# Kernel optimization log

Measured on AMD Instinct MI355X. Metric: run time of the kernel, lower is better.

Reference implementation:

```python
import jax, jax.numpy as jnp
import numpy as np

# CPC 'same'-mode InfoNCE loss. encoded_x/context: [S, B, L] (steps, batch, latent).
# predictor(context, k) is modeled as a per-k linear map with weight Wk[k] of shape [L, L]
# (y = x @ Wk[k].T), the standard CPC prediction head.

def setup_inputs() -> dict:
    key = jax.random.key(0)
    k1, k2, k3 = jax.random.split(key, 3)
    S, B, L, K = 128, 256, 512, 8
    encoded_x = jax.random.normal(k1, (S, B, L), dtype=jnp.float32)
    context = jax.random.normal(k2, (S, B, L), dtype=jnp.float32)
    Wk = jax.random.normal(k3, (K, L, L), dtype=jnp.float32) * (1.0 / np.sqrt(L))
    return {
        "encoded_x": encoded_x,
        "context": context,
        "Wk": Wk,
        "timesteps_in": 16,
        "timesteps_out": 8,
        "timesteps_ignore": 0,
    }


def reference(encoded_x, context, Wk, timesteps_in, timesteps_out, timesteps_ignore):
    S, B, L = encoded_x.shape
    K = timesteps_out
    # number of inner 'step' iterations: context[T_in : -(K + ignore + 1)]
    steps = S - timesteps_in - (K + timesteps_ignore + 1)
    ctx = context[timesteps_in:timesteps_in + steps]            # [steps, B, L]
    # predictor for all k at once: pred[k, s, b, :] = ctx[s, b] @ Wk[k].T
    pred = jnp.einsum('sbl,kml->ksbm', ctx, Wk)                 # [K, steps, B, L]
    # encoded_latent for each k: encoded_x[T_in + k + 1 : T_in + k + 1 + steps]
    idx = timesteps_in + 1 + jnp.arange(K)[:, None] + jnp.arange(steps)[None, :]
    enc = encoded_x[idx]                                        # [K, steps, B, L]
    # sim[k, s, b, c] = <enc[k,s,b], pred[k,s,c]>  (== mm(enc, pred.T) per (k, step))
    sim = jnp.einsum('ksbl,kscl->ksbc', enc, pred)              # [K, steps, B, B]
    logp = jax.nn.log_softmax(sim, axis=-1)                     # LogSoftmax(dim=-1)
    # loss: sum of diagonals, normalized by -(B * K * steps)
    diag_sum = jnp.einsum('ksbb->', logp)
    denom = B * K * steps
    loss = diag_sum / (-1.0 * denom)
    # correct: argmax over dim 0 (rows, enc axis) per column == arange(B)
    pred_cls = jnp.argmax(logp, axis=2)                         # [K, steps, B]
    correct = jnp.sum(pred_cls == jnp.arange(B)[None, None, :])
    accuracy = correct.astype(jnp.float32) / denom
    return (accuracy, loss)
```

## Files before the change

### kernel.cpp

```cpp
#include <hip/hip_runtime.h>
#include <math.h>
#include <stdint.h>

#define S_DIM 128
#define B_DIM 256
#define L_DIM 512
#define K_DIM 8
#define T_IN  16
#define STEPS 103
#define DENOM (K_DIM * STEPS * B_DIM)
#define PRED_K ((size_t)STEPS * B_DIM * L_DIM)

typedef __attribute__((ext_vector_type(8))) short short8;
typedef __attribute__((ext_vector_type(4))) float f32x4;

__device__ __forceinline__ short f2bf(float f) {
    unsigned u = __float_as_uint(f);
    u += 0x7FFFu + ((u >> 16) & 1u);
    return (short)(u >> 16);
}

__device__ __forceinline__ void load_lds16(const void* g, void* l) {
    __builtin_amdgcn_global_load_lds(
        (const __attribute__((address_space(1))) unsigned*)g,
        (__attribute__((address_space(3))) unsigned*)l, 16, 0, 0);
}

#define ENC4 ((S_DIM * B_DIM * L_DIM) / 4)
#define CTX4 ((STEPS * B_DIM * L_DIM) / 4)
#define WK4  ((K_DIM * L_DIM * L_DIM) / 4)
#define CV_N (ENC4 + CTX4 + WK4)
#define Z_N  (DENOM + 2)
__global__ void convert_all(const float* __restrict__ enc_in, const float* __restrict__ ctx_in,
                            const float* __restrict__ wk_in, short* __restrict__ enc_out,
                            short* __restrict__ ctx_out, short* __restrict__ wk_out,
                            unsigned long long* __restrict__ zbuf) {
    for (int i = blockIdx.x * blockDim.x + threadIdx.x; i < CV_N + Z_N;
         i += gridDim.x * blockDim.x) {
        if (i >= CV_N) { zbuf[i - CV_N] = 0ull; continue; }
        const float4* src; short4* dst; int j;
        if (i < ENC4)             { src = (const float4*)enc_in; dst = (short4*)enc_out; j = i; }
        else if (i < ENC4 + CTX4) { src = (const float4*)ctx_in; dst = (short4*)ctx_out; j = i - ENC4; }
        else                      { src = (const float4*)wk_in;  dst = (short4*)wk_out;  j = i - ENC4 - CTX4; }
        const float4 v = src[j];
        short4 o;
        o.x = f2bf(v.x); o.y = f2bf(v.y); o.z = f2bf(v.z); o.w = f2bf(v.w);
        dst[j] = o;
    }
}

__global__ __launch_bounds__(256)
void gemm_bf16(const short* __restrict__ A, const short* __restrict__ W,
               short* __restrict__ C) {
    __shared__ short As[128 * 64];
    __shared__ short Bs[128 * 64];
    const int gx  = gridDim.x;
    const int nwg = gx * gridDim.y;
    const int id  = blockIdx.y * gx + blockIdx.x;
    const int q8 = nwg >> 3, r8 = nwg & 7;
    const int xcd = id & 7;
    const int lin = (xcd < r8 ? xcd * (q8 + 1) : r8 * (q8 + 1) + (xcd - r8) * q8)
                  + (id >> 3);
    const int lgx = 31 - __clz(gx);
    const int bm = lin >> lgx;
    const int xc = lin & (gx - 1);
    const int kin = xc >> 2, cn = xc & 3;

    const int t = threadIdx.x;
    const int w = t >> 6, lane = t & 63, quad = lane >> 4, l15 = lane & 15;
    const int wm = w & 1, wn = w >> 1;
    const int rl8 = lane >> 3, ch8 = lane & 7;

    const short* Ab = A + (size_t)bm * 128 * L_DIM;
    const short* Wb = W + ((size_t)kin * L_DIM + cn * 128) * L_DIM;
    short* Ck = C + kin * PRED_K;

    f32x4 acc[4][4] = {};

    for (int kt = 0; kt < L_DIM; kt += 64) {
        #pragma unroll
        for (int q = 0; q < 4; q++) {
            const int rb = w * 32 + q * 8;
            const int row = rb + rl8;
            const int ch = ch8 ^ (row & 7);
            load_lds16(Ab + (size_t)row * L_DIM + kt + ch * 8, &As[rb * 64]);
            load_lds16(Wb + (size_t)row * L_DIM + kt + ch * 8, &Bs[rb * 64]);
        }
        __syncthreads();
        #pragma unroll
        for (int k2 = 0; k2 < 2; k2++) {
            short8 a[4], b[4];
            #pragma unroll
            for (int i = 0; i < 4; i++) {
                const int m = wm * 64 + i * 16 + l15;
                a[i] = *(const short8*)&As[m * 64 + ((k2 * 4 + quad) ^ (m & 7)) * 8];
                const int n = wn * 64 + i * 16 + l15;
                b[i] = *(const short8*)&Bs[n * 64 + ((k2 * 4 + quad) ^ (n & 7)) * 8];
            }
            #pragma unroll
            for (int i = 0; i < 4; i++)
                #pragma unroll
                for (int j = 0; j < 4; j++)
                    acc[i][j] = __builtin_amdgcn_mfma_f32_16x16x32_bf16(a[i], b[j], acc[i][j], 0, 0, 0);
        }
        __syncthreads();
    }
    #pragma unroll
    for (int i = 0; i < 4; i++)
        #pragma unroll
        for (int r = 0; r < 4; r++) {
            const int row = bm * 128 + wm * 64 + i * 16 + quad * 4 + r;
            short* Cr = Ck + (size_t)row * L_DIM + cn * 128 + wn * 64 + l15;
            #pragma unroll
            for (int j = 0; j < 4; j++)
                Cr[j * 16] = f2bf(acc[i][j][r]);
        }
}

__global__ __launch_bounds__(512, 2)
void sim_phase(const short* __restrict__ encbf, const short* __restrict__ pred,
               const int k0, unsigned long long* __restrict__ col_best,
               float* __restrict__ diag_accum) {
    __shared__ short Es[2][256 * 64];
    __shared__ short Ps[2][256 * 64];
    __shared__ float rmx[256][2];
    __shared__ float rsx[256][2];
    __shared__ float dred[8];
    const int s = blockIdx.x, kin = blockIdx.y;
    const int k = k0 + kin;
    const int t = threadIdx.x, w = t >> 6, lane = t & 63;
    const int quad = lane >> 4, l15 = lane & 15;
    const int wm = w & 3, wn = w >> 2;
    const int rl8 = lane >> 3, ch8 = lane & 7;

    const short* Eb = encbf + ((size_t)(T_IN + 1 + k + s) * B_DIM) * L_DIM;
    const short* Pb = pred + kin * PRED_K + (size_t)s * B_DIM * L_DIM;

    const short* esrc[4]; const short* psrc[4]; int rdst[4];
    #pragma unroll
    for (int q = 0; q < 4; q++) {
        const int rb = w * 32 + q * 8, row = rb + rl8;
        const int co = (ch8 ^ (row & 7)) * 8;
        esrc[q] = Eb + (size_t)row * L_DIM + co;
        psrc[q] = Pb + (size_t)row * L_DIM + co;
        rdst[q] = rb * 64;
    }

    #pragma unroll
    for (int q = 0; q < 4; q++) load_lds16(esrc[q], &Es[0][rdst[q]]);
    #pragma unroll
    for (int q = 0; q < 4; q++) load_lds16(psrc[q], &Ps[0][rdst[q]]);
    __syncthreads();

    f32x4 acc[4][8] = {};
    int cur = 0;
    #pragma unroll
    for (int kt = 0; kt < L_DIM; kt += 64) {
        if (kt + 64 < L_DIM) {
            #pragma unroll
            for (int q = 0; q < 4; q++)
                load_lds16(esrc[q] + kt + 64, &Es[cur ^ 1][rdst[q]]);
            #pragma unroll
            for (int q = 0; q < 4; q++)
                load_lds16(psrc[q] + kt + 64, &Ps[cur ^ 1][rdst[q]]);
        }
        #pragma unroll
        for (int k2 = 0; k2 < 2; k2++) {
            short8 a[4], b[8];
            #pragma unroll
            for (int i = 0; i < 4; i++) {
                const int m = wm * 64 + i * 16 + l15;
                a[i] = *(const short8*)&Es[cur][m * 64 + ((k2 * 4 + quad) ^ (m & 7)) * 8];
            }
            #pragma unroll
            for (int j = 0; j < 8; j++) {
                const int n = wn * 128 + j * 16 + l15;
                b[j] = *(const short8*)&Ps[cur][n * 64 + ((k2 * 4 + quad) ^ (n & 7)) * 8];
            }
            #pragma unroll
            for (int i = 0; i < 4; i++)
                #pragma unroll
                for (int j = 0; j < 8; j++)
                    acc[i][j] = __builtin_amdgcn_mfma_f32_16x16x32_bf16(a[i], b[j], acc[i][j], 0, 0, 0);
        }
        __syncthreads();
        cur ^= 1;
    }

    float rm[4][4];
    #pragma unroll
    for (int i = 0; i < 4; i++)
        #pragma unroll
        for (int r = 0; r < 4; r++) {
            float m = acc[i][0][r];
            #pragma unroll
            for (int j = 1; j < 8; j++) m = fmaxf(m, acc[i][j][r]);
            rm[i][r] = m;
        }
    #pragma unroll
    for (int off = 1; off < 16; off <<= 1)
        #pragma unroll
        for (int i = 0; i < 4; i++)
            #pragma unroll
            for (int r = 0; r < 4; r++)
                rm[i][r] = fmaxf(rm[i][r], __shfl_xor(rm[i][r], off, 64));
    if (l15 == 0)
        #pragma unroll
        for (int i = 0; i < 4; i++)
            #pragma unroll
            for (int r = 0; r < 4; r++)
                rmx[wm * 64 + i * 16 + quad * 4 + r][wn] = rm[i][r];
    __syncthreads();

    float mrow[4][4];
    #pragma unroll
    for (int i = 0; i < 4; i++)
        #pragma unroll
        for (int r = 0; r < 4; r++) {
            const float2 v = *(const float2*)rmx[wm * 64 + i * 16 + quad * 4 + r];
            mrow[i][r] = fmaxf(v.x, v.y);
        }

    float rs[4][4];
    #pragma unroll
    for (int i = 0; i < 4; i++)
        #pragma unroll
        for (int r = 0; r < 4; r++) {
            float sum = 0.f;
            #pragma unroll
            for (int j = 0; j < 8; j++) sum += __expf(acc[i][j][r] - mrow[i][r]);
            rs[i][r] = sum;
        }
    #pragma unroll
    for (int off = 1; off < 16; off <<= 1)
        #pragma unroll
        for (int i = 0; i < 4; i++)
            #pragma unroll
            for (int r = 0; r < 4; r++)
                rs[i][r] += __shfl_xor(rs[i][r], off, 64);
    if (l15 == 0)
        #pragma unroll
        for (int i = 0; i < 4; i++)
            #pragma unroll
            for (int r = 0; r < 4; r++)
                rsx[wm * 64 + i * 16 + quad * 4 + r][wn] = rs[i][r];
    __syncthreads();

    float lse[4][4];
    #pragma unroll
    for (int i = 0; i < 4; i++)
        #pragma unroll
        for (int r = 0; r < 4; r++) {
            const float2 v = *(const float2*)rsx[wm * 64 + i * 16 + quad * 4 + r];
            lse[i][r] = mrow[i][r] + __logf(v.x + v.y);
        }

    #pragma unroll
    for (int j = 0; j < 8; j++) {
        unsigned long long best = 0;
        #pragma unroll
        for (int i = 0; i < 4; i++)
            #pragma unroll
            for (int r = 0; r < 4; r++) {
                const int grow = wm * 64 + i * 16 + quad * 4 + r;
                const float v = acc[i][j][r] - lse[i][r];
                unsigned int fb = __float_as_uint(v);
                fb = (fb & 0x80000000u) ? ~fb : (fb | 0x80000000u);
                const unsigned long long p =
                    ((unsigned long long)fb << 32) | (unsigned long long)(255 - grow);
                if (p > best) best = p;
            }
        unsigned long long o;
        o = __shfl_xor(best, 16, 64); if (o > best) best = o;
        o = __shfl_xor(best, 32, 64); if (o > best) best = o;
        if (quad == 0)
            atomicMax(&col_best[((size_t)k * STEPS + s) * B_DIM + wn * 128 + j * 16 + l15], best);
    }

    {
        float dv = 0.f;
        #pragma unroll
        for (int i = 0; i < 4; i++)
            #pragma unroll
            for (int j = 0; j < 8; j++)
                #pragma unroll
                for (int r = 0; r < 4; r++) {
                    const int grow = wm * 64 + i * 16 + quad * 4 + r;
                    const int c = wn * 128 + j * 16 + l15;
                    if (grow == c) dv += acc[i][j][r] - lse[i][r];
                }
        #pragma unroll
        for (int off = 1; off < 64; off <<= 1) dv += __shfl_xor(dv, off, 64);
        if (lane == 0) dred[w] = dv;
    }
    __syncthreads();
    if (t == 0) {
        float dv = 0.f;
        #pragma unroll
        for (int i = 0; i < 8; i++) dv += dred[i];
        atomicAdd(diag_accum, dv);
    }
}

__global__ void count_finalize(const unsigned long long* __restrict__ col_best,
                               int* __restrict__ correct_accum,
                               float* __restrict__ diag_accum,
                               unsigned int* __restrict__ done,
                               float* __restrict__ out) {
    __shared__ int red[256];
    const int t = threadIdx.x;
    int cnt = 0;
    for (int i = blockIdx.x * 256 + t; i < DENOM; i += gridDim.x * 256) {
        const int c = i & (B_DIM - 1);
        const int b = 255 - (int)(col_best[i] & 0xFFFFFFFFull);
        cnt += (b == c) ? 1 : 0;
    }
    red[t] = cnt;
    __syncthreads();
    for (int off = 128; off > 0; off >>= 1) {
        if (t < off) red[t] += red[t + off];
        __syncthreads();
    }
    if (t == 0) {
        atomicAdd(correct_accum, red[0]);
        __threadfence();
        if (atomicAdd(done, 1u) == gridDim.x - 1) {
            const int   c = atomicAdd(correct_accum, 0);
            const float d = atomicAdd(diag_accum, 0.0f);
            const float denom = (float)DENOM;
            out[0] = (float)c / denom;
            out[1] = -d / denom;
        }
    }
}

extern "C" void kernel_launch(void* const* d_in, const int* in_sizes, int n_in,
                              void* d_out, int out_size, void* d_ws, size_t ws_size,
                              hipStream_t stream) {
    const float* encoded_x = (const float*)d_in[0];
    const float* context   = (const float*)d_in[1];
    const float* Wk        = (const float*)d_in[2];
    float* out = (float*)d_out;

    const size_t enc_elems = (size_t)S_DIM * B_DIM * L_DIM;
    const size_t ctx_elems = (size_t)STEPS * B_DIM * L_DIM;
    const size_t wk_elems  = (size_t)K_DIM * L_DIM * L_DIM;
    const size_t pred_k_bytes = ctx_elems * 2;

    char* ws = (char*)d_ws;
    short* encbf = (short*)ws;
    short* ctxbf = (short*)(ws + enc_elems * 2);
    short* wkbf  = (short*)(ws + (enc_elems + ctx_elems) * 2);
    const size_t off = (enc_elems + ctx_elems + wk_elems) * 2;
    unsigned long long* col_best = (unsigned long long*)(ws + off);
    float* diag_accum    = (float*)(ws + off + (size_t)DENOM * 8);
    int*   correct_accum = (int*)  (ws + off + (size_t)DENOM * 8 + 4);
    unsigned int* done   = (unsigned int*)(ws + off + (size_t)DENOM * 8 + 8);
    const size_t fixed = off + (size_t)DENOM * 8 + 64;
    short* pred = (short*)(ws + fixed);

    int g = K_DIM;
    while (g > 1 && fixed + (size_t)g * pred_k_bytes > ws_size) g >>= 1;

    convert_all<<<2048, 256, 0, stream>>>(encoded_x, context + (size_t)T_IN * B_DIM * L_DIM,
                                          Wk, encbf, ctxbf, wkbf, col_best);

    const dim3 g1(4 * g, (STEPS * B_DIM) / 128);
    const dim3 g2(STEPS, g);
    for (int k0 = 0; k0 < K_DIM; k0 += g) {
        gemm_bf16<<<g1, 256, 0, stream>>>(ctxbf, wkbf + (size_t)k0 * L_DIM * L_DIM, pred);
        sim_phase<<<g2, 512, 0, stream>>>(encbf, pred, k0, col_best, diag_accum);
    }
    count_finalize<<<64, 256, 0, stream>>>(col_best, correct_accum, diag_accum, done, out);
}
```

Baseline: 422.6 us.

## Enlarge pred GEMM tiles with double buffering and fuse accuracy count into sim kernel

The predictor GEMM moves from 128x128 tiles with 256 threads to 256x256 tiles with 512 threads, double-buffered LDS and prefetch of the next K slice, so each tile gets more operand reuse and load latency overlaps with MFMA work. The per-column argmax is now reduced in shared memory inside sim_phase and counted directly into an accuracy counter. This removes the large col_best global buffer, its zeroing and the separate count pass. The trade-off is higher register and LDS use in the GEMM, which may reduce occupancy, and fewer workgroups in the GEMM grid.

```diff
diff --git a/kernel.cpp b/kernel.cpp
--- a/kernel.cpp
+++ b/kernel.cpp
@@ -30,7 +30,7 @@
 #define CTX4 ((STEPS * B_DIM * L_DIM) / 4)
 #define WK4  ((K_DIM * L_DIM * L_DIM) / 4)
 #define CV_N (ENC4 + CTX4 + WK4)
-#define Z_N  (DENOM + 2)
+#define Z_N  2
 __global__ void convert_all(const float* __restrict__ enc_in, const float* __restrict__ ctx_in,
                             const float* __restrict__ wk_in, short* __restrict__ enc_out,
                             short* __restrict__ ctx_out, short* __restrict__ wk_out,
@@ -49,11 +49,11 @@
     }
 }
 
-__global__ __launch_bounds__(256)
+__global__ __launch_bounds__(512, 2)
 void gemm_bf16(const short* __restrict__ A, const short* __restrict__ W,
                short* __restrict__ C) {
-    __shared__ short As[128 * 64];
-    __shared__ short Bs[128 * 64];
+    __shared__ short As[2][256 * 64];
+    __shared__ short Bs[2][256 * 64];
     const int gx  = gridDim.x;
     const int nwg = gx * gridDim.y;
     const int id  = blockIdx.y * gx + blockIdx.x;
@@ -64,68 +64,89 @@
     const int lgx = 31 - __clz(gx);
     const int bm = lin >> lgx;
     const int xc = lin & (gx - 1);
-    const int kin = xc >> 2, cn = xc & 3;
+    const int kin = xc >> 1, cn = xc & 1;
 
     const int t = threadIdx.x;
     const int w = t >> 6, lane = t & 63, quad = lane >> 4, l15 = lane & 15;
-    const int wm = w & 1, wn = w >> 1;
+    const int wm = w & 3, wn = w >> 2;
     const int rl8 = lane >> 3, ch8 = lane & 7;
 
-    const short* Ab = A + (size_t)bm * 128 * L_DIM;
-    const short* Wb = W + ((size_t)kin * L_DIM + cn * 128) * L_DIM;
+    const short* Ab = A + (size_t)bm * 256 * L_DIM;
+    const short* Wb = W + ((size_t)kin * L_DIM + cn * 256) * L_DIM;
     short* Ck = C + kin * PRED_K;
 
-    f32x4 acc[4][4] = {};
-
+    const short* asrc[4]; const short* bsrc[4]; int rdst[4];
+    #pragma unroll
+    for (int q = 0; q < 4; q++) {
+        const int rb = w * 32 + q * 8, row = rb + rl8;
+        const int co = (ch8 ^ (row & 7)) * 8;
+        asrc[q] = Ab + (size_t)row * L_DIM + co;
+        bsrc[q] = Wb + (size_t)row * L_DIM + co;
+        rdst[q] = rb * 64;
+    }
+
+    #pragma unroll
+    for (int q = 0; q < 4; q++) load_lds16(asrc[q], &As[0][rdst[q]]);
+    #pragma unroll
+    for (int q = 0; q < 4; q++) load_lds16(bsrc[q], &Bs[0][rdst[q]]);
+    __syncthreads();
+
+    f32x4 acc[4][8] = {};
+    int cur = 0;
+    #pragma unroll
     for (int kt = 0; kt < L_DIM; kt += 64) {
-        #pragma unroll
-        for (int q = 0; q < 4; q++) {
-            const int rb = w * 32 + q * 8;
-            const int row = rb + rl8;
-            const int ch = ch8 ^ (row & 7);
-            load_lds16(Ab + (size_t)row * L_DIM + kt + ch * 8, &As[rb * 64]);
-            load_lds16(Wb + (size_t)row * L_DIM + kt + ch * 8, &Bs[rb * 64]);
-        }
-        __syncthreads();
+        if (kt + 64 < L_DIM) {
+            #pragma unroll
+            for (int q = 0; q < 4; q++)
+                load_lds16(asrc[q] + kt + 64, &As[cur ^ 1][rdst[q]]);
+            #pragma unroll
+            for (int q = 0; q < 4; q++)
+                load_lds16(bsrc[q] + kt + 64, &Bs[cur ^ 1][rdst[q]]);
+        }
         #pragma unroll
         for (int k2 = 0; k2 < 2; k2++) {
-            short8 a[4], b[4];
+            short8 a[4], b[8];
             #pragma unroll
             for (int i = 0; i < 4; i++) {
                 const int m = wm * 64 + i * 16 + l15;
-                a[i] = *(const short8*)&As[m * 64 + ((k2 * 4 + quad) ^ (m & 7)) * 8];
-                const int n = wn * 64 + i * 16 + l15;
-                b[i] = *(const short8*)&Bs[n * 64 + ((k2 * 4 + quad) ^ (n & 7)) * 8];
+                a[i] = *(const short8*)&As[cur][m * 64 + ((k2 * 4 + quad) ^ (m & 7)) * 8];
+            }
+            #pragma unroll
+            for (int j = 0; j < 8; j++) {
+                const int n = wn * 128 + j * 16 + l15;
+                b[j] = *(const short8*)&Bs[cur][n * 64 + ((k2 * 4 + quad) ^ (n & 7)) * 8];
             }
             #pragma unroll
             for (int i = 0; i < 4; i++)
                 #pragma unroll
-                for (int j = 0; j < 4; j++)
+                for (int j = 0; j < 8; j++)
                     acc[i][j] = __builtin_amdgcn_mfma_f32_16x16x32_bf16(a[i], b[j], acc[i][j], 0, 0, 0);
         }
         __syncthreads();
-    }
-    #pragma unroll
-    for (int i = 0; i < 4; i++)
-        #pragma unroll
-        for (int r = 0; r < 4; r++) {
-            const int row = bm * 128 + wm * 64 + i * 16 + quad * 4 + r;
-            short* Cr = Ck + (size_t)row * L_DIM + cn * 128 + wn * 64 + l15;
-            #pragma unroll
-            for (int j = 0; j < 4; j++)
+        cur ^= 1;
+    }
+    #pragma unroll
+    for (int i = 0; i < 4; i++)
+        #pragma unroll
+        for (int r = 0; r < 4; r++) {
+            const int row = bm * 256 + wm * 64 + i * 16 + quad * 4 + r;
+            short* Cr = Ck + (size_t)row * L_DIM + cn * 256 + wn * 128 + l15;
+            #pragma unroll
+            for (int j = 0; j < 8; j++)
                 Cr[j * 16] = f2bf(acc[i][j][r]);
         }
 }
 
 __global__ __launch_bounds__(512, 2)
 void sim_phase(const short* __restrict__ encbf, const short* __restrict__ pred,
-               const int k0, unsigned long long* __restrict__ col_best,
+               const int k0, int* __restrict__ correct_accum,
                float* __restrict__ diag_accum) {
     __shared__ short Es[2][256 * 64];
     __shared__ short Ps[2][256 * 64];
     __shared__ float rmx[256][2];
     __shared__ float rsx[256][2];
     __shared__ float dred[8];
+    __shared__ unsigned long long cbest[256][4];
     const int s = blockIdx.x, kin = blockIdx.y;
     const int k = k0 + kin;
     const int t = threadIdx.x, w = t >> 6, lane = t & 63;
@@ -273,8 +294,18 @@
         unsigned long long o;
         o = __shfl_xor(best, 16, 64); if (o > best) best = o;
         o = __shfl_xor(best, 32, 64); if (o > best) best = o;
-        if (quad == 0)
-            atomicMax(&col_best[((size_t)k * STEPS + s) * B_DIM + wn * 128 + j * 16 + l15], best);
+        if (quad == 0) cbest[wn * 128 + j * 16 + l15][wm] = best;
+    }
+    __syncthreads();
+    if (t < 256) {
+        const unsigned long long* cb = cbest[t];
+        unsigned long long best = cb[0];
+        if (cb[1] > best) best = cb[1];
+        if (cb[2] > best) best = cb[2];
+        if (cb[3] > best) best = cb[3];
+        const int b = 255 - (int)(best & 0xFFFFFFFFull);
+        const unsigned long long m = __ballot(b == t);
+        if (lane == 0) atomicAdd(correct_accum, (int)__popcll(m));
     }
 
     {
@@ -302,36 +333,12 @@
     }
 }
 
-__global__ void count_finalize(const unsigned long long* __restrict__ col_best,
-                               int* __restrict__ correct_accum,
-                               float* __restrict__ diag_accum,
-                               unsigned int* __restrict__ done,
-                               float* __restrict__ out) {
-    __shared__ int red[256];
-    const int t = threadIdx.x;
-    int cnt = 0;
-    for (int i = blockIdx.x * 256 + t; i < DENOM; i += gridDim.x * 256) {
-        const int c = i & (B_DIM - 1);
-        const int b = 255 - (int)(col_best[i] & 0xFFFFFFFFull);
-        cnt += (b == c) ? 1 : 0;
-    }
-    red[t] = cnt;
-    __syncthreads();
-    for (int off = 128; off > 0; off >>= 1) {
-        if (t < off) red[t] += red[t + off];
-        __syncthreads();
-    }
-    if (t == 0) {
-        atomicAdd(correct_accum, red[0]);
-        __threadfence();
-        if (atomicAdd(done, 1u) == gridDim.x - 1) {
-            const int   c = atomicAdd(correct_accum, 0);
-            const float d = atomicAdd(diag_accum, 0.0f);
-            const float denom = (float)DENOM;
-            out[0] = (float)c / denom;
-            out[1] = -d / denom;
-        }
-    }
+__global__ void finalize(const int* __restrict__ correct_accum,
+                         const float* __restrict__ diag_accum,
+                         float* __restrict__ out) {
+    const float denom = (float)DENOM;
+    out[0] = (float)(*correct_accum) / denom;
+    out[1] = -(*diag_accum) / denom;
 }
 
 extern "C" void kernel_launch(void* const* d_in, const int* in_sizes, int n_in,
@@ -352,24 +359,23 @@
     short* ctxbf = (short*)(ws + enc_elems * 2);
     short* wkbf  = (short*)(ws + (enc_elems + ctx_elems) * 2);
     const size_t off = (enc_elems + ctx_elems + wk_elems) * 2;
-    unsigned long long* col_best = (unsigned long long*)(ws + off);
-    float* diag_accum    = (float*)(ws + off + (size_t)DENOM * 8);
-    int*   correct_accum = (int*)  (ws + off + (size_t)DENOM * 8 + 4);
-    unsigned int* done   = (unsigned int*)(ws + off + (size_t)DENOM * 8 + 8);
-    const size_t fixed = off + (size_t)DENOM * 8 + 64;
+    float* diag_accum    = (float*)(ws + off);
+    int*   correct_accum = (int*)  (ws + off + 4);
+    const size_t fixed = off + 64;
     short* pred = (short*)(ws + fixed);
 
     int g = K_DIM;
     while (g > 1 && fixed + (size_t)g * pred_k_bytes > ws_size) g >>= 1;
 
     convert_all<<<2048, 256, 0, stream>>>(encoded_x, context + (size_t)T_IN * B_DIM * L_DIM,
-                                          Wk, encbf, ctxbf, wkbf, col_best);
-
-    const dim3 g1(4 * g, (STEPS * B_DIM) / 128);
+                                          Wk, encbf, ctxbf, wkbf,
+                                          (unsigned long long*)diag_accum);
+
+    const dim3 g1(2 * g, 103);
     const dim3 g2(STEPS, g);
     for (int k0 = 0; k0 < K_DIM; k0 += g) {
-        gemm_bf16<<<g1, 256, 0, stream>>>(ctxbf, wkbf + (size_t)k0 * L_DIM * L_DIM, pred);
-        sim_phase<<<g2, 512, 0, stream>>>(encbf, pred, k0, col_best, diag_accum);
-    }
-    count_finalize<<<64, 256, 0, stream>>>(col_best, correct_accum, diag_accum, done, out);
-}
+        gemm_bf16<<<g1, 512, 0, stream>>>(ctxbf, wkbf + (size_t)k0 * L_DIM * L_DIM, pred);
+        sim_phase<<<g2, 512, 0, stream>>>(encbf, pred, k0, correct_accum, diag_accum);
+    }
+    finalize<<<1, 1, 0, stream>>>(correct_accum, diag_accum, out);
+}
```

After: 440.5 us. +4.2%, slower.
